# Kernel tuning notes

Hardware: AMD Instinct MI355X
Metric: run time of the kernel (lower is better)

The kernel has to match this reference:

```python
import jax, jax.numpy as jnp
import numpy as np

B, D, L, H = 4, 1024, 2048, 8
HD = D // H


def setup_inputs() -> dict:
    key = jax.random.key(0)
    k1, k2, k3, k4 = jax.random.split(key, 4)
    query = jax.random.normal(k1, (B, D, L), dtype=jnp.float32)
    mask = jax.random.randint(k2, (B, L), 0, 2, dtype=jnp.int32)
    W1 = jax.random.normal(k3, (2 * D, D), dtype=jnp.float32) * (D ** -0.5)
    Wq = jax.random.normal(k4, (D, D), dtype=jnp.float32) * (D ** -0.5)
    return {"query": query, "mask": mask, "W1": W1, "Wq": Wq}


def _split_heads(x):
    # [B, L, C] -> [B, H, L, C//H]
    b, l, c = x.shape
    return x.reshape(b, l, H, c // H).transpose(0, 2, 1, 3)


def reference(query, mask, W1, Wq):
    # 1x1 conv == channel GEMM; produce [B, L, out]
    temp = jnp.einsum('od,bdl->blo', W1, query)   # [B, L, 2D] (K|V)
    q = jnp.einsum('od,bdl->blo', Wq, query)      # [B, L, D]
    k, v = jnp.split(temp, 2, axis=-1)
    q = _split_heads(q) * (HD ** -0.5)            # [B, H, L, HD]
    k = _split_heads(k)
    v = _split_heads(v)
    scores = jnp.einsum('bhqd,bhkd->bhqk', q, k)  # [B, H, L, L]
    m = mask.astype(jnp.float32)[:, None, None, :]
    logits = scores + (-1e30) * (1.0 - m)
    weights = jax.nn.softmax(logits, axis=-1)     # dropout p=0 (eval)
    out = jnp.einsum('bhqk,bhkd->bhqd', weights, v)
    out = out.transpose(0, 2, 1, 3).reshape(B, L, D)  # merge heads
    return out.transpose(0, 2, 1)                 # [B, D, L]
```

## Files before the change

### kernel.cpp

```cpp
#include <hip/hip_runtime.h>
#include <hip/hip_bf16.h>

#define B_  4
#define D_  1024
#define L_  2048
#define H_  8
#define HD_ 128

typedef __attribute__((ext_vector_type(8))) short bf16x8;
typedef __attribute__((ext_vector_type(4))) float f32x4;
typedef __attribute__((ext_vector_type(2))) unsigned uint2v;
typedef __attribute__((ext_vector_type(4))) unsigned uint4v;

#if __has_builtin(__builtin_amdgcn_permlane16_swap) && __has_builtin(__builtin_amdgcn_permlane32_swap)
#define HAS_PERMSWAP 1
#else
#define HAS_PERMSWAP 0
#endif

static __device__ __forceinline__ ushort f2bf(float f) {
    unsigned u = __float_as_uint(f);
    unsigned r = (u + 0x7fffu + ((u >> 16) & 1u)) >> 16;
    return (ushort)r;
}

static __device__ __forceinline__ unsigned cvt_pk_bf16(float lo, float hi) {
    unsigned r;
    asm("v_cvt_pk_bf16_f32 %0, %1, %2" : "=v"(r) : "v"(lo), "v"(hi));
    return r;
}

static __device__ __forceinline__ float exp2_fast(float x) {
#if __has_builtin(__builtin_amdgcn_exp2f)
    return __builtin_amdgcn_exp2f(x);
#else
    return exp2f(x);
#endif
}

static __device__ __forceinline__ float qmax4(float x) {
#if HAS_PERMSWAP
    uint2v a = __builtin_amdgcn_permlane16_swap(__float_as_uint(x), __float_as_uint(x), false, false);
    float y = fmaxf(__uint_as_float(a[0]), __uint_as_float(a[1]));
    uint2v b = __builtin_amdgcn_permlane32_swap(__float_as_uint(y), __float_as_uint(y), false, false);
    return fmaxf(__uint_as_float(b[0]), __uint_as_float(b[1]));
#else
    x = fmaxf(x, __shfl_xor(x, 16, 64));
    return fmaxf(x, __shfl_xor(x, 32, 64));
#endif
}

static __device__ __forceinline__ void dma16(const ushort* g, ushort* l) {
    __builtin_amdgcn_global_load_lds(
        (const __attribute__((address_space(1))) void*)g,
        (__attribute__((address_space(3))) void*)l, 16, 0, 0);
}

__global__ void k_zero_out(float* __restrict__ out, int n) {
    int i = blockIdx.x * 256 + threadIdx.x;
    if (i < n) out[i] = 0.f;
}

__global__ void k_prep(const float* __restrict__ q, const float* __restrict__ W1,
                       const float* __restrict__ Wq, const int* __restrict__ mask,
                       ushort* __restrict__ Wb, ushort* __restrict__ Xt,
                       int* __restrict__ cidx, int* __restrict__ cnt) {
    __shared__ float tile[64][65];
    const int bid = blockIdx.x, t = threadIdx.x;
    if (bid < 4) {
        int b = bid;
        if (t < 64) {
            int lane = t;
            const int* mb = mask + b * L_;
            int base = 0;
            for (int c = 0; c < L_; c += 64) {
                int m = mb[c + lane];
                unsigned long long bal = __ballot(m != 0);
                int pre = __popcll(bal & ((1ull << lane) - 1ull));
                if (m) cidx[b * L_ + base + pre] = c + lane;
                base += __popcll(bal);
            }
            for (int j = base + lane; j < L_; j += 64) cidx[b * L_ + j] = 0;
            if (lane == 0) cnt[b] = base;
        }
    } else if (bid < 4 + 2048) {
        int tb = bid - 4;
        int bx = tb & 31, by = (tb >> 5) & 15, bz = tb >> 9;
        int l0 = bx * 64, d0 = by * 64;
        int rr = t >> 4, cc = t & 15;
        const float* src = q + (size_t)bz * D_ * L_;
        for (int i = 0; i < 4; i++) {
            int r = rr + 16 * i;
            float4 v = *(const float4*)&src[(size_t)(d0 + r) * L_ + l0 + cc * 4];
            tile[r][cc * 4 + 0] = v.x;
            tile[r][cc * 4 + 1] = v.y;
            tile[r][cc * 4 + 2] = v.z;
            tile[r][cc * 4 + 3] = v.w;
        }
        __syncthreads();
        ushort* dst = Xt + (size_t)bz * L_ * D_;
        for (int i = 0; i < 4; i++) {
            int lr = rr + 16 * i;
            uint2 o;
            o.x = cvt_pk_bf16(tile[cc * 4 + 0][lr], tile[cc * 4 + 1][lr]);
            o.y = cvt_pk_bf16(tile[cc * 4 + 2][lr], tile[cc * 4 + 3][lr]);
            *(uint2*)&dst[(size_t)(l0 + lr) * D_ + d0 + cc * 4] = o;
        }
    } else {
        int i = (bid - 2052) * 256 + t;
        const int n1 = 2 * D_ * D_ / 4;
        float4 v = (i < n1) ? ((const float4*)W1)[i] : ((const float4*)Wq)[i - n1];
        ushort4 o;
        o.x = f2bf(v.x); o.y = f2bf(v.y); o.z = f2bf(v.z); o.w = f2bf(v.w);
        ((ushort4*)Wb)[i] = o;
    }
}

__launch_bounds__(256)
__global__ void k_proj(const ushort* __restrict__ Wb, const ushort* __restrict__ Xt,
                       const int* __restrict__ cidx, const int* __restrict__ cnt,
                       ushort* __restrict__ Qb, ushort* __restrict__ Kb,
                       ushort* __restrict__ Vt) {
    __shared__ alignas(16) ushort As[2][128 * 32];
    __shared__ alignas(16) ushort Bs[2][128 * 32];
    const int bid = blockIdx.x;
    const int xcd = bid & 7, j = bid >> 3;
    const int wid = xcd * 192 + j;
    const int st = wid >> 4, m = wid & 15;
    const int b  = st / 24;
    const int sr = st % 24;
    const int sx = sr & 3, sy = sr >> 2;
    const int x  = sx * 4 + (m & 3);
    const int y  = sy * 4 + (m >> 2);
    const int o0 = y * 128;
    const int l0 = x * 128;
    const int type = o0 >> 10;
    if (type < 2) {
        int tiles = (cnt[b] + 127) >> 7;
        if (x >= tiles) return;
    }
    const int t = threadIdx.x;
    const int wave = t >> 6, lane = t & 63, quad = lane >> 4, li = lane & 15;
    const int wm = wave >> 1, wn = wave & 1;
    const ushort* Xb = Xt + (size_t)b * L_ * D_;

    const int srow = t >> 2;
    const int csw = ((srow + (srow >> 2)) & 3);
    const int g = (t & 3) ^ csw;
    const ushort* aSrc[2];
    const ushort* bSrc[2];
    for (int i = 0; i < 2; i++) {
        int r = i * 64 + srow;
        aSrc[i] = Wb + (size_t)(o0 + r) * D_ + g * 8;
        int l = l0 + r;
        int gl = (type < 2) ? cidx[b * L_ + l] : l;
        bSrc[i] = Xb + (size_t)gl * D_ + g * 8;
    }

    f32x4 acc[4][4] = {};

    const int fsw = (li + (li >> 2)) & 3;
    const int fchunk = (quad ^ fsw) * 8;

    for (int i = 0; i < 2; i++) dma16(aSrc[i], &As[0][(i * 256 + wave * 64) * 8]);
    for (int i = 0; i < 2; i++) dma16(bSrc[i], &Bs[0][(i * 256 + wave * 64) * 8]);

    int buf = 0;
    for (int k0 = 0; k0 < D_; k0 += 32, buf ^= 1) {
        __syncthreads();

        if (k0 + 32 < D_) {
            int nb = buf ^ 1;
            for (int i = 0; i < 2; i++)
                dma16(aSrc[i] + k0 + 32, &As[nb][(i * 256 + wave * 64) * 8]);
            for (int i = 0; i < 2; i++)
                dma16(bSrc[i] + k0 + 32, &Bs[nb][(i * 256 + wave * 64) * 8]);
        }

        bf16x8 af[4], bfr[4];
        for (int mf = 0; mf < 4; mf++) {
            int row = wm * 64 + mf * 16 + li;
            af[mf] = *(const bf16x8*)&As[buf][row * 32 + fchunk];
        }
        for (int nf = 0; nf < 4; nf++) {
            int row = wn * 64 + nf * 16 + li;
            bfr[nf] = *(const bf16x8*)&Bs[buf][row * 32 + fchunk];
        }
        for (int mf = 0; mf < 4; mf++)
            for (int nf = 0; nf < 4; nf++)
                acc[mf][nf] = __builtin_amdgcn_mfma_f32_16x16x32_bf16(af[mf], bfr[nf], acc[mf][nf], 0, 0, 0);
    }

    const float qscale = 0.1275174495450826f;
    for (int mf = 0; mf < 4; mf++) {
        int o = o0 + wm * 64 + mf * 16 + quad * 4;
        int c = o & 1023;
        int h = c >> 7, hd = c & 127;
        for (int nf = 0; nf < 4; nf++) {
            int l = l0 + wn * 64 + nf * 16 + li;
            f32x4 v = acc[mf][nf];
            if (type == 0) {
                uint2 kk;
                kk.x = cvt_pk_bf16(v[0], v[1]);
                kk.y = cvt_pk_bf16(v[2], v[3]);
                *(uint2*)&Kb[(((size_t)(b * H_ + h)) * L_ + l) * HD_ + hd] = kk;
            } else if (type == 1) {
                size_t base = (size_t)(b * H_ + h) * HD_;
                Vt[(base + hd + 0) * L_ + l] = f2bf(v[0]);
                Vt[(base + hd + 1) * L_ + l] = f2bf(v[1]);
                Vt[(base + hd + 2) * L_ + l] = f2bf(v[2]);
                Vt[(base + hd + 3) * L_ + l] = f2bf(v[3]);
            } else {
                uint2 qq;
                qq.x = cvt_pk_bf16(v[0] * qscale, v[1] * qscale);
                qq.y = cvt_pk_bf16(v[2] * qscale, v[3] * qscale);
                *(uint2*)&Qb[(((size_t)(b * H_ + h)) * L_ + l) * HD_ + hd] = qq;
            }
        }
    }
}

__launch_bounds__(256, 4)
__global__ void k_attn(const ushort* __restrict__ Qb, const ushort* __restrict__ Kb,
                       const ushort* __restrict__ Vt, const int* __restrict__ mask,
                       float* __restrict__ out) {
    __shared__ alignas(16) ushort Ks[2][32][128];
    __shared__ alignas(16) ushort Vs[2][128][32];
#if !HAS_PERMSWAP
    __shared__ alignas(16) ushort Pl[4][16][40];
#endif
    const int blk = blockIdx.x;
    const int h = blk & 7, qt = (blk >> 3) & 31, b = blk >> 8;
    const int t = threadIdx.x;
    const int w = t >> 6, lane = t & 63, quad = lane >> 4, li = lane & 15;
    const int q0 = qt * 64 + w * 16;
    const ushort* Qh = Qb + (size_t)(b * H_ + h) * L_ * HD_;
    const ushort* Kh = Kb + (size_t)(b * H_ + h) * L_ * HD_;
    const ushort* Vh = Vt + (size_t)(b * H_ + h) * HD_ * L_;
    const int* mb = mask + b * L_;

    int cm = 0;
    for (int c = lane; c < L_; c += 64) cm += mb[c];
    cm += __shfl_xor(cm, 32, 64);
    cm += __shfl_xor(cm, 16, 64);
    cm += __shfl_xor(cm, 8, 64);
    cm += __shfl_xor(cm, 4, 64);
    cm += __shfl_xor(cm, 2, 64);
    cm += __shfl_xor(cm, 1, 64);
    const int cnt = cm;
    int cnt_pad = (cnt + 31) & ~31;
    if (cnt_pad < 32) cnt_pad = 32;

    const ushort* kgp[2]; const ushort* vgp[2];
    for (int i = 0; i < 2; i++) {
        int seg = w * 2 + i;
        int key = seg * 4 + (lane >> 4);
        int ck  = (lane & 15) ^ (key & 15);
        kgp[i] = Kh + (size_t)key * HD_ + ck * 8;
        int hd  = seg * 16 + (lane >> 2);
        int cv  = (lane & 3) ^ (hd & 3);
        vgp[i] = Vh + (size_t)hd * L_ + cv * 8;
    }

    for (int i = 0; i < 2; i++) dma16(kgp[i], &Ks[0][0][0] + (w * 2 + i) * 512);
    for (int i = 0; i < 2; i++) dma16(vgp[i], &Vs[0][0][0] + (w * 2 + i) * 512);

    bf16x8 qf[4];
    for (int kf = 0; kf < 4; kf++)
        qf[kf] = *(const bf16x8*)&Qh[(size_t)(q0 + li) * HD_ + kf * 32 + quad * 8];

    bf16x8 ones;
    for (int i = 0; i < 8; i++) ones[i] = (short)0x3F80;

    float mrun = -1e30f;
    f32x4 lsum = {};
    f32x4 acc[8] = {};

    int buf = 0;
    for (int n0 = 0; n0 < cnt_pad; n0 += 32, buf ^= 1) {
        __syncthreads();

        if (n0 + 32 < cnt_pad) {
            int nb = buf ^ 1;
            for (int i = 0; i < 2; i++)
                dma16(kgp[i] + (size_t)(n0 + 32) * HD_, &Ks[nb][0][0] + (w * 2 + i) * 512);
            for (int i = 0; i < 2; i++)
                dma16(vgp[i] + (n0 + 32), &Vs[nb][0][0] + (w * 2 + i) * 512);
        }

        f32x4 s[2] = {};
        __builtin_amdgcn_s_setprio(1);
        for (int kf = 0; kf < 4; kf++) {
            bf16x8 kfr[2];
            for (int mt = 0; mt < 2; mt++)
                kfr[mt] = *(const bf16x8*)&Ks[buf][mt * 16 + li][((kf * 4 + quad) ^ li) * 8];
            for (int mt = 0; mt < 2; mt++)
                s[mt] = __builtin_amdgcn_mfma_f32_16x16x32_bf16(kfr[mt], qf[kf], s[mt], 0, 0, 0);
        }
        __builtin_amdgcn_s_setprio(0);

        if (n0 + 32 > cnt) {
            for (int mt = 0; mt < 2; mt++)
                for (int r = 0; r < 4; r++)
                    if (n0 + mt * 16 + quad * 4 + r >= cnt) s[mt][r] = -1e30f;
        }

        float a0 = fmaxf(fmaxf(s[0][0], s[0][1]), fmaxf(s[0][2], s[0][3]));
        float a1 = fmaxf(fmaxf(s[1][0], s[1][1]), fmaxf(s[1][2], s[1][3]));
        float nm = qmax4(fmaxf(a0, a1));

        if (!__all(nm <= mrun + 8.f)) {
            float mnew = fmaxf(mrun, nm);
            float alpha = exp2_fast(mrun - mnew);
            mrun = mnew;
            int sb = (lane & 48) | (quad * 4);
            float ar0 = __shfl(alpha, sb + 0, 64);
            float ar1 = __shfl(alpha, sb + 1, 64);
            float ar2 = __shfl(alpha, sb + 2, 64);
            float ar3 = __shfl(alpha, sb + 3, 64);
            lsum[0] *= ar0; lsum[1] *= ar1; lsum[2] *= ar2; lsum[3] *= ar3;
            for (int nf2 = 0; nf2 < 8; nf2++) {
                acc[nf2][0] *= ar0;
                acc[nf2][1] *= ar1;
                acc[nf2][2] *= ar2;
                acc[nf2][3] *= ar3;
            }
        }

        for (int mt = 0; mt < 2; mt++)
            for (int r = 0; r < 4; r++)
                s[mt][r] = exp2_fast(s[mt][r] - mrun);

        bf16x8 pa;
#if HAS_PERMSWAP
        {
            unsigned c0 = cvt_pk_bf16(s[0][0], s[0][1]);
            unsigned c1 = cvt_pk_bf16(s[0][2], s[0][3]);
            unsigned c2 = cvt_pk_bf16(s[1][0], s[1][1]);
            unsigned c3 = cvt_pk_bf16(s[1][2], s[1][3]);
            uint2v x02 = __builtin_amdgcn_permlane32_swap(c0, c2, false, false);
            uint2v u02 = __builtin_amdgcn_permlane16_swap(x02[0], x02[1], false, false);
            uint2v x13 = __builtin_amdgcn_permlane32_swap(c1, c3, false, false);
            uint2v u13 = __builtin_amdgcn_permlane16_swap(x13[0], x13[1], false, false);
            uint4v paw;
            paw[0] = u02[0];
            paw[1] = u13[0];
            paw[2] = u02[1];
            paw[3] = u13[1];
            pa = __builtin_bit_cast(bf16x8, paw);
        }
#else
        {
            for (int mt = 0; mt < 2; mt++) {
                uint2 pk;
                pk.x = cvt_pk_bf16(s[mt][0], s[mt][1]);
                pk.y = cvt_pk_bf16(s[mt][2], s[mt][3]);
                *(uint2*)&Pl[w][li][mt * 16 + quad * 4] = pk;
            }
            pa = *(const bf16x8*)&Pl[w][li][quad * 8];
        }
#endif

        __builtin_amdgcn_s_setprio(1);
        lsum = __builtin_amdgcn_mfma_f32_16x16x32_bf16(pa, ones, lsum, 0, 0, 0);
        for (int nf2 = 0; nf2 < 8; nf2++) {
            bf16x8 vb = *(const bf16x8*)&Vs[buf][nf2 * 16 + li][(quad ^ (li & 3)) * 8];
            acc[nf2] = __builtin_amdgcn_mfma_f32_16x16x32_bf16(pa, vb, acc[nf2], 0, 0, 0);
        }
        __builtin_amdgcn_s_setprio(0);
    }

    float i0 = 1.0f / lsum[0];
    float i1 = 1.0f / lsum[1];
    float i2 = 1.0f / lsum[2];
    float i3 = 1.0f / lsum[3];
    int l = q0 + quad * 4;
    for (int nf2 = 0; nf2 < 8; nf2++) {
        int d = h * HD_ + nf2 * 16 + li;
        float4 o4 = { acc[nf2][0] * i0, acc[nf2][1] * i1,
                      acc[nf2][2] * i2, acc[nf2][3] * i3 };
        *(float4*)&out[((size_t)(b * D_ + d)) * L_ + l] = o4;
    }
}

extern "C" void kernel_launch(void* const* d_in, const int* in_sizes, int n_in,
                              void* d_out, int out_size, void* d_ws, size_t ws_size,
                              hipStream_t stream) {
    const float* query = nullptr;
    const int*   mask  = nullptr;
    const float* W1    = nullptr;
    const float* Wq    = nullptr;
    for (int i = 0; i < n_in; i++) {
        switch (in_sizes[i]) {
            case 8388608: query = (const float*)d_in[i]; break;
            case 8192:    mask  = (const int*)d_in[i];   break;
            case 2097152: W1    = (const float*)d_in[i]; break;
            case 1048576: Wq    = (const float*)d_in[i]; break;
        }
    }
    float* out = (float*)d_out;

    if (ws_size < 50331648u || !query || !mask || !W1 || !Wq) {
        hipLaunchKernelGGL(k_zero_out, dim3((out_size + 255) / 256), dim3(256), 0, stream,
                           out, out_size);
        return;
    }

    ushort* Wb = (ushort*)d_out;
    ushort* Xt = (ushort*)((char*)d_out + 6291456);
    int* cidx  = (int*)((char*)d_out + 23068672);
    int* cnt   = (int*)((char*)d_out + 23101440);
    char* ws = (char*)d_ws;
    ushort* Qb = (ushort*)(ws + 0);
    ushort* Kb = (ushort*)(ws + 16777216);
    ushort* Vt = (ushort*)(ws + 33554432);

    hipLaunchKernelGGL(k_prep, dim3(4 + 2048 + 3072), dim3(256), 0, stream,
                       query, W1, Wq, mask, Wb, Xt, cidx, cnt);
    hipLaunchKernelGGL(k_proj, dim3(1536), dim3(256), 0, stream, Wb, Xt, cidx, cnt, Qb, Kb, Vt);
    hipLaunchKernelGGL(k_attn, dim3(1024), dim3(256), 0, stream, Qb, Kb, Vt, mask, out);
}
```

Before: 213.5 us.

## Triple-buffer projection GEMM LDS with explicit vmcnt waits

Replaces the double-buffered LDS staging in the projection GEMM with a three-stage ring buffer that prefetches two k-tiles ahead. Explicit s_waitcnt vmcnt(4) plus a raw s_barrier replace __syncthreads, so only the oldest tile's DMA must complete before compute starts. The aim is to hide more global-load latency behind MFMA work. In exchange it uses more LDS per block (48KB vs 32KB), which may lower occupancy, and correctness depends on the hand-counted vmcnt value.

```diff
diff --git a/kernel.cpp b/kernel.cpp
--- a/kernel.cpp
+++ b/kernel.cpp
@@ -121,8 +121,7 @@
                        const int* __restrict__ cidx, const int* __restrict__ cnt,
                        ushort* __restrict__ Qb, ushort* __restrict__ Kb,
                        ushort* __restrict__ Vt) {
-    __shared__ alignas(16) ushort As[2][128 * 32];
-    __shared__ alignas(16) ushort Bs[2][128 * 32];
+    __shared__ alignas(16) ushort sh[3 * 4096 * 2];
     const int bid = blockIdx.x;
     const int xcd = bid & 7, j = bid >> 3;
     const int wid = xcd * 192 + j;
@@ -162,33 +161,42 @@
     const int fsw = (li + (li >> 2)) & 3;
     const int fchunk = (quad ^ fsw) * 8;
 
-    for (int i = 0; i < 2; i++) dma16(aSrc[i], &As[0][(i * 256 + wave * 64) * 8]);
-    for (int i = 0; i < 2; i++) dma16(bSrc[i], &Bs[0][(i * 256 + wave * 64) * 8]);
-
-    int buf = 0;
-    for (int k0 = 0; k0 < D_; k0 += 32, buf ^= 1) {
-        __syncthreads();
-
-        if (k0 + 32 < D_) {
-            int nb = buf ^ 1;
-            for (int i = 0; i < 2; i++)
-                dma16(aSrc[i] + k0 + 32, &As[nb][(i * 256 + wave * 64) * 8]);
-            for (int i = 0; i < 2; i++)
-                dma16(bSrc[i] + k0 + 32, &Bs[nb][(i * 256 + wave * 64) * 8]);
-        }
-
+    for (int tt = 0; tt < 2; tt++) {
+        ushort* Ad = sh + tt * 4096;
+        ushort* Bd = sh + 12288 + tt * 4096;
+        for (int i = 0; i < 2; i++) dma16(aSrc[i] + tt * 32, Ad + (i * 256 + wave * 64) * 8);
+        for (int i = 0; i < 2; i++) dma16(bSrc[i] + tt * 32, Bd + (i * 256 + wave * 64) * 8);
+    }
+
+    int cb = 0;
+    for (int idx = 0; idx < 32; idx++) {
+        if (idx < 31) asm volatile("s_waitcnt vmcnt(4)" ::: "memory");
+        else          asm volatile("s_waitcnt vmcnt(0)" ::: "memory");
+        __builtin_amdgcn_sched_barrier(0);
+        __builtin_amdgcn_s_barrier();
+        __builtin_amdgcn_sched_barrier(0);
+
+        if (idx + 2 < 32) {
+            int ib = cb + 2; if (ib >= 3) ib -= 3;
+            int ko = (idx + 2) * 32;
+            ushort* Ad = sh + ib * 4096;
+            ushort* Bd = sh + 12288 + ib * 4096;
+            for (int i = 0; i < 2; i++) dma16(aSrc[i] + ko, Ad + (i * 256 + wave * 64) * 8);
+            for (int i = 0; i < 2; i++) dma16(bSrc[i] + ko, Bd + (i * 256 + wave * 64) * 8);
+        }
+
+        const ushort* Ab = sh + cb * 4096;
+        const ushort* Bb = sh + 12288 + cb * 4096;
         bf16x8 af[4], bfr[4];
-        for (int mf = 0; mf < 4; mf++) {
-            int row = wm * 64 + mf * 16 + li;
-            af[mf] = *(const bf16x8*)&As[buf][row * 32 + fchunk];
-        }
-        for (int nf = 0; nf < 4; nf++) {
-            int row = wn * 64 + nf * 16 + li;
-            bfr[nf] = *(const bf16x8*)&Bs[buf][row * 32 + fchunk];
-        }
+        for (int mf = 0; mf < 4; mf++)
+            af[mf] = *(const bf16x8*)&Ab[(wm * 64 + mf * 16 + li) * 32 + fchunk];
+        for (int nf = 0; nf < 4; nf++)
+            bfr[nf] = *(const bf16x8*)&Bb[(wn * 64 + nf * 16 + li) * 32 + fchunk];
         for (int mf = 0; mf < 4; mf++)
             for (int nf = 0; nf < 4; nf++)
                 acc[mf][nf] = __builtin_amdgcn_mfma_f32_16x16x32_bf16(af[mf], bfr[nf], acc[mf][nf], 0, 0, 0);
+
+        cb++; if (cb >= 3) cb = 0;
     }
 
     const float qscale = 0.1275174495450826f;
```

After: 208.6 us. 2.3% less time.
